# Kernel tuning notes

Measured on AMD Instinct MI355X. Metric: run time of the kernel, lower is better.

## Reference

```python
import jax, jax.numpy as jnp
import numpy as np

N, D = 8192, 256
NUM_CLASSES = 128
MARGIN = 0.2


def setup_inputs() -> dict:
    key = jax.random.key(0)
    k1, k2 = jax.random.split(key)
    embeddings = jax.random.normal(k1, (N, D), dtype=jnp.float32)
    labels = jax.random.randint(k2, (N,), 0, NUM_CLASSES, dtype=jnp.int64)
    return {"embeddings": embeddings, "labels": labels}


def reference(embeddings, labels):
    n = embeddings.shape[0]
    # cosine distance matrix: 1 - cos_sim, clipped to [0, 2]
    norm = jnp.sqrt(jnp.sum(embeddings * embeddings, axis=-1, keepdims=True))
    normed = embeddings / jnp.maximum(norm, 1e-12)
    sim = normed @ normed.T                      # (N, N)
    dist = jnp.clip(1.0 - sim, 0.0, 2.0)

    same = labels[:, None] == labels[None, :]    # (N, N) same-class mask
    eye = jnp.eye(n, dtype=bool)
    cand = same & ~eye                           # valid positives per anchor
    valid = cand.any(axis=1)                     # anchors with >=1 positive
    pos_idx = jnp.argmax(cand, axis=1)           # first same-class index != i

    rows = jnp.arange(n)
    d_ap = dist[rows, pos_idx]                   # (N,)

    # semi-hard mining: negatives with d_ap < d < d_ap + margin, fallback hardest
    neg = ~same                                  # different class (self excluded)
    semi = neg & (dist > d_ap[:, None]) & (dist < d_ap[:, None] + MARGIN)
    has_semi = semi.any(axis=1)
    inf = jnp.asarray(jnp.inf, dist.dtype)
    d_semi = jnp.where(semi, dist, inf)
    d_hard = jnp.where(neg, dist, inf)
    neg_idx = jnp.where(has_semi, jnp.argmin(d_semi, axis=1), jnp.argmin(d_hard, axis=1))

    d_an = dist[rows, neg_idx]
    losses = jnp.maximum(d_ap - d_an + MARGIN, 0.0) * valid.astype(dist.dtype)
    cnt = valid.sum().astype(dist.dtype)
    return jnp.where(cnt > 0, losses.sum() / cnt, jnp.zeros((), dist.dtype))
```

## Files before the change

### kernel.cpp

```cpp
#include <hip/hip_runtime.h>
#include <math.h>

#define NN 8192
#define DD 256
#define MARGIN 0.2f
#define SL 16
#define CPS (NN / SL)
#define TILES (CPS / 128)
#define IMAX 0x7fffffff

typedef __attribute__((ext_vector_type(4))) float f32x4;
typedef __attribute__((ext_vector_type(2))) long long2_t;
typedef unsigned int u32;
typedef unsigned short u16;
typedef unsigned char u8;

static __device__ __forceinline__ u8 f2e4m3(float x) {
    float a = fabsf(x);
    a = fminf(a, 448.0f);
    const u32 s = (__float_as_uint(x) >> 31) << 7;
    if (a < 0.015625f) {
        const int m = (int)rintf(a * 512.0f);
        return (u8)(s | m);
    }
    u32 u = __float_as_uint(a);
    u += 0x7FFFF + ((u >> 20) & 1);
    const u32 e = (u >> 23) - 120;
    return (u8)(s | (e << 3) | ((u >> 20) & 7));
}

#define GLOAD16(g, l)                                                             \
    __builtin_amdgcn_global_load_lds(                                             \
        (const __attribute__((address_space(1))) void*)(g),                       \
        (__attribute__((address_space(3))) void*)(l), 16, 0, 0)

static __device__ __forceinline__ void comb2(int& a1, int& a2, int b1, int b2) {
    const int lo = min(a1, b1);
    const int hi = max(a1, b1);
    a2 = min(hi, min(a2, b2));
    a1 = lo;
}

__global__ void kprepclass(const float* __restrict__ emb, const int* __restrict__ labels,
                           u8* __restrict__ E8, float* __restrict__ invn,
                           int* __restrict__ posidx) {
    const int tid = threadIdx.x;
    if (blockIdx.x < 2048) {
        const int wid = tid >> 6, l = tid & 63;
        const int row = blockIdx.x * 4 + wid;
        const float4 v = *(const float4*)&emb[(size_t)row * DD + l * 4];
        float ss = v.x * v.x + v.y * v.y + v.z * v.z + v.w * v.w;
#pragma unroll
        for (int o = 1; o < 64; o <<= 1) ss += __shfl_xor(ss, o);
        const float inv = 1.0f / fmaxf(sqrtf(ss), 1e-12f);
        if (l == 0) invn[row] = inv;
        const u32 b0 = f2e4m3(v.x * inv), b1 = f2e4m3(v.y * inv);
        const u32 b2 = f2e4m3(v.z * inv), b3 = f2e4m3(v.w * inv);
        const u32 packed = b0 | (b1 << 8) | (b2 << 16) | (b3 << 24);
        const int kc = l >> 4, h = (l >> 3) & 1, c = (l >> 1) & 3, o = (l & 1) * 4;
        const int g = kc * 64 + c * 16 + h * 8 + o;
        *(u32*)&E8[(size_t)row * DD + g] = packed;
    } else {
        const int c = blockIdx.x - 2048;
        int m1 = IMAX, m2 = IMAX;
        for (int j = tid; j < NN; j += 256) {
            if (labels[j] == c) {
                if (m1 == IMAX) m1 = j;
                else if (m2 == IMAX) m2 = j;
            }
        }
#pragma unroll
        for (int o = 1; o < 64; o <<= 1)
            comb2(m1, m2, __shfl_xor(m1, o), __shfl_xor(m2, o));
        __shared__ int s1[4], s2[4];
        __shared__ int bj1, bj2;
        const int wave = tid >> 6, lane = tid & 63;
        if (lane == 0) { s1[wave] = m1; s2[wave] = m2; }
        __syncthreads();
        if (tid == 0) {
            comb2(m1, m2, s1[1], s2[1]);
            comb2(m1, m2, s1[2], s2[2]);
            comb2(m1, m2, s1[3], s2[3]);
            bj1 = m1; bj2 = m2;
        }
        __syncthreads();
        const int j1 = bj1, j2 = bj2;
        for (int j = tid; j < NN; j += 256)
            if (labels[j] == c) posidx[j] = (j2 == IMAX) ? -1 : ((j == j1) ? j2 : j1);
    }
}

__global__ void kdap(const float* __restrict__ emb, const float* __restrict__ invn,
                     const int* __restrict__ posidx, float* __restrict__ dap) {
    const int wid = threadIdx.x >> 6, l = threadIdx.x & 63;
    const int i = blockIdx.x * 4 + wid;
    const int p = posidx[i];
    float dv = 0.0f;
    if (p >= 0) {
        const float4 a = *(const float4*)&emb[(size_t)i * DD + l * 4];
        const float4 b = *(const float4*)&emb[(size_t)p * DD + l * 4];
        float s = a.x * b.x + a.y * b.y + a.z * b.z + a.w * b.w;
#pragma unroll
        for (int o = 1; o < 64; o <<= 1) s += __shfl_xor(s, o);
        const float sim = s * invn[i] * invn[p];
        dv = fminf(fmaxf(1.0f - sim, 0.0f), 2.0f);
    }
    if (l == 0) dap[i] = dv;
}

__global__ __launch_bounds__(256) void kmine(
    const u8* __restrict__ E8, const int* __restrict__ labels,
    const float* __restrict__ dap, float* __restrict__ pM1, float* __restrict__ pMN)
{
    __shared__ __align__(16) u8 At0[128 * 256], At1[128 * 256];
    __shared__ __align__(16) int Ls[CPS];
    __shared__ float RedN[2][128], RedS[2][128];

    const int tid = threadIdx.x;
    const int l = tid & 63;
    const int wid = tid >> 6;
    const int wr = wid >> 1;
    const int wc = wid & 1;
    const int slice = blockIdx.x;
    const int a0 = blockIdx.y * 128;

    const int frow = l & 15;
    const int fq = l >> 4;

    if (tid < 128) {
        const int4 lv = *(const int4*)&labels[slice * CPS + tid * 4];
        *(int4*)&Ls[tid * 4] = lv;
    }
    int la[4]; float hiv[4];
#pragma unroll
    for (int n = 0; n < 4; ++n) {
        const int ai = a0 + wc * 64 + n * 16 + frow;
        la[n] = labels[ai];
        hiv[n] = 1.0f - dap[ai];
    }
    const char* Ec = (const char*)E8;
    long2_t breg[4][4];
#pragma unroll
    for (int n = 0; n < 4; ++n)
#pragma unroll
        for (int kc = 0; kc < 4; ++kc)
            breg[n][kc] = *(const long2_t*)(Ec +
                (size_t)(a0 + wc * 64 + n * 16 + frow) * 256 + kc * 64 + fq * 16);

    const char* asrc = Ec + ((size_t)(slice * CPS) + (tid >> 4)) * 256
                          + (((tid & 15) ^ (tid >> 4)) * 16);

#define STAGE(BUF, OFF) do {                                    \
        _Pragma("unroll")                                       \
        for (int i = 0; i < 8; ++i)                             \
            GLOAD16(asrc + (OFF) + i * 4096,                    \
                    &BUF[tid * 16 + i * 4096]);                 \
    } while (0)

    float mN[4], m1[4];
#pragma unroll
    for (int n = 0; n < 4; ++n) { mN[n] = -INFINITY; m1[n] = -INFINITY; }
    const f32x4 Zv = {0.f, 0.f, 0.f, 0.f};
    f32x4 acc[4][4];

#define COMPTILE(BUF, T) do {                                                       \
        _Pragma("unroll")                                                           \
        for (int kc = 0; kc < 4; ++kc) {                                            \
            long2_t a2[4];                                                          \
            _Pragma("unroll")                                                       \
            for (int m = 0; m < 4; ++m)                                             \
                a2[m] = *(const long2_t*)&BUF[(wr * 64 + m * 16 + frow) * 256       \
                                              + ((4 * kc + fq) ^ frow) * 16];      \
            __builtin_amdgcn_s_setprio(1);                                          \
            _Pragma("unroll")                                                       \
            for (int m = 0; m < 4; ++m)                                             \
                _Pragma("unroll")                                                   \
                for (int n = 0; n < 4; ++n)                                         \
                    acc[m][n] = __builtin_amdgcn_mfma_f32_16x16x32_fp8_fp8(         \
                        a2[m].x, breg[n][kc].x, (kc == 0) ? Zv : acc[m][n],         \
                        0, 0, 0);                                                   \
            _Pragma("unroll")                                                       \
            for (int m = 0; m < 4; ++m)                                             \
                _Pragma("unroll")                                                   \
                for (int n = 0; n < 4; ++n)                                         \
                    acc[m][n] = __builtin_amdgcn_mfma_f32_16x16x32_fp8_fp8(         \
                        a2[m].y, breg[n][kc].y, acc[m][n], 0, 0, 0);                \
            __builtin_amdgcn_s_setprio(0);                                          \
        }                                                                           \
        {                                                                           \
            int lcv[16];                                                            \
            _Pragma("unroll")                                                       \
            for (int m = 0; m < 4; ++m) {                                           \
                const int4 v = *(const int4*)&Ls[(T) * 128 + wr * 64 + m * 16       \
                                                 + fq * 4];                        \
                lcv[m * 4 + 0] = v.x; lcv[m * 4 + 1] = v.y;                         \
                lcv[m * 4 + 2] = v.z; lcv[m * 4 + 3] = v.w;                         \
            }                                                                       \
            _Pragma("unroll")                                                       \
            for (int n = 0; n < 4; ++n) {                                           \
                _Pragma("unroll")                                                   \
                for (int m = 0; m < 4; ++m)                                         \
                    _Pragma("unroll")                                               \
                    for (int r = 0; r < 4; ++r) {                                   \
                        const float sv = acc[m][n][r];                              \
                        const float sel = (lcv[m * 4 + r] != la[n]) ? sv            \
                                                                    : -INFINITY;    \
                        mN[n] = fmaxf(mN[n], sel);                                  \
                        m1[n] = fmaxf(m1[n], (sel < hiv[n]) ? sel : -INFINITY);     \
                    }                                                               \
            }                                                                       \
        }                                                                           \
    } while (0)

    STAGE(At0, 0);
    asm volatile("s_waitcnt lgkmcnt(0)" ::: "memory");

    STAGE(At1, 32768);
    asm volatile("s_waitcnt vmcnt(8)" ::: "memory");
    __builtin_amdgcn_s_barrier();
    COMPTILE(At0, 0);
    __builtin_amdgcn_s_barrier();
    STAGE(At0, 65536);
    asm volatile("s_waitcnt vmcnt(8)" ::: "memory");
    __builtin_amdgcn_s_barrier();
    COMPTILE(At1, 1);
    __builtin_amdgcn_s_barrier();
    STAGE(At1, 98304);
    asm volatile("s_waitcnt vmcnt(8)" ::: "memory");
    __builtin_amdgcn_s_barrier();
    COMPTILE(At0, 2);
    __builtin_amdgcn_s_barrier();
    asm volatile("s_waitcnt vmcnt(0)" ::: "memory");
    __builtin_amdgcn_s_barrier();
    COMPTILE(At1, 3);
#undef STAGE
#undef COMPTILE

#pragma unroll
    for (int n = 0; n < 4; ++n) {
        mN[n] = fmaxf(mN[n], __shfl_xor(mN[n], 16));
        mN[n] = fmaxf(mN[n], __shfl_xor(mN[n], 32));
        m1[n] = fmaxf(m1[n], __shfl_xor(m1[n], 16));
        m1[n] = fmaxf(m1[n], __shfl_xor(m1[n], 32));
    }
    __builtin_amdgcn_s_barrier();
    if (fq == 0) {
#pragma unroll
        for (int n = 0; n < 4; ++n) {
            RedN[wr][wc * 64 + n * 16 + frow] = mN[n];
            RedS[wr][wc * 64 + n * 16 + frow] = m1[n];
        }
    }
    __syncthreads();
    if (tid < 128) {
        pMN[slice * NN + a0 + tid] = fmaxf(RedN[0][tid], RedN[1][tid]);
        pM1[slice * NN + a0 + tid] = fmaxf(RedS[0][tid], RedS[1][tid]);
    }
}

__global__ void kcombine(const int* __restrict__ posidx, const float* __restrict__ dap,
                         const float* __restrict__ pM1, const float* __restrict__ pMN,
                         float* __restrict__ partials)
{
    const int i = blockIdx.x * 256 + threadIdx.x;
    float loss = 0.0f, cnt = 0.0f;
    if (posidx[i] >= 0) {
        float s1 = -INFINITY, sN = -INFINITY;
#pragma unroll
        for (int s = 0; s < SL; ++s) {
            s1 = fmaxf(s1, pM1[s * NN + i]);
            sN = fmaxf(sN, pMN[s * NN + i]);
        }
        const float da = dap[i];
        const float lo = 1.0f - da - MARGIN;
        const float M = (s1 > lo) ? s1 : sN;
        const float dan = fminf(fmaxf(1.0f - M, 0.0f), 2.0f);
        loss = fmaxf(da - dan + MARGIN, 0.0f);
        cnt = 1.0f;
    }
#pragma unroll
    for (int off = 1; off < 64; off <<= 1) {
        loss += __shfl_xor(loss, off);
        cnt  += __shfl_xor(cnt, off);
    }
    __shared__ float sl[4], sc[4];
    const int wave = threadIdx.x >> 6, lane = threadIdx.x & 63;
    if (lane == 0) { sl[wave] = loss; sc[wave] = cnt; }
    __syncthreads();
    if (threadIdx.x == 0) {
        partials[blockIdx.x]      = sl[0] + sl[1] + sl[2] + sl[3];
        partials[32 + blockIdx.x] = sc[0] + sc[1] + sc[2] + sc[3];
    }
}

__global__ void kfinal(const float* __restrict__ partials, float* __restrict__ out) {
    const int t = threadIdx.x;
    float L = (t < 32) ? partials[t] : 0.0f;
    float C = (t < 32) ? partials[32 + t] : 0.0f;
#pragma unroll
    for (int off = 1; off < 64; off <<= 1) {
        L += __shfl_xor(L, off);
        C += __shfl_xor(C, off);
    }
    if (t == 0) out[0] = (C > 0.0f) ? (L / C) : 0.0f;
}

extern "C" void kernel_launch(void* const* d_in, const int* in_sizes, int n_in,
                              void* d_out, int out_size, void* d_ws, size_t ws_size,
                              hipStream_t stream) {
    const float* emb  = (const float*)d_in[0];
    const int* labels = (const int*)d_in[1];
    float* out = (float*)d_out;

    char* w = (char*)d_ws;
    u8*    E8   = (u8*)w;                        w += (size_t)NN * DD;
    float* invn = (float*)w;                     w += NN * 4;
    float* dapv = (float*)w;                     w += NN * 4;
    int*   posi = (int*)w;                       w += NN * 4;
    float* pM1  = (float*)w;                     w += (size_t)SL * NN * 4;
    float* pMN  = (float*)w;                     w += (size_t)SL * NN * 4;
    float* parts = (float*)w;

    kprepclass<<<2048 + 128, 256, 0, stream>>>(emb, labels, E8, invn, posi);
    kdap<<<NN / 4, 256, 0, stream>>>(emb, invn, posi, dapv);
    kmine<<<dim3(SL, NN / 128), 256, 0, stream>>>(E8, labels, dapv, pM1, pMN);
    kcombine<<<NN / 256, 256, 0, stream>>>(posi, dapv, pM1, pMN, parts);
    kfinal<<<1, 64, 0, stream>>>(parts, out);
}
```

Before: 58.17 us.

## Use 16x16x128 scaled FP8 MFMA and fold final reduction into combine kernel

Replaces the pairs of 16x16x32 FP8 MFMAs with a single MX-scaled 16x16x128 f8f6f4 MFMA per K half, using unit scales. To feed the wider operands it drops the interleaved E8 layout for a plain row layout and loads 32 contiguous bytes per operand. It also removes the separate final-reduction launch: the last combine block to finish, detected with an atomic counter, performs the final sum. This cuts MFMA instruction count and one kernel launch, but needs a counter reset in the prep kernel and changes the LDS read pattern.

```diff
diff --git a/kernel.cpp b/kernel.cpp
--- a/kernel.cpp
+++ b/kernel.cpp
@@ -11,8 +11,8 @@
 
 typedef __attribute__((ext_vector_type(4))) float f32x4;
 typedef __attribute__((ext_vector_type(2))) long long2_t;
+typedef __attribute__((ext_vector_type(8))) int i32x8;
 typedef unsigned int u32;
-typedef unsigned short u16;
 typedef unsigned char u8;
 
 static __device__ __forceinline__ u8 f2e4m3(float x) {
@@ -29,6 +29,12 @@
     return (u8)(s | (e << 3) | ((u >> 20) & 7));
 }
 
+static __device__ __forceinline__ i32x8 pack8(long2_t lo, long2_t hi) {
+    union { long2_t l2[2]; i32x8 v; } u;
+    u.l2[0] = lo; u.l2[1] = hi;
+    return u.v;
+}
+
 #define GLOAD16(g, l)                                                             \
     __builtin_amdgcn_global_load_lds(                                             \
         (const __attribute__((address_space(1))) void*)(g),                       \
@@ -43,7 +49,7 @@
 
 __global__ void kprepclass(const float* __restrict__ emb, const int* __restrict__ labels,
                            u8* __restrict__ E8, float* __restrict__ invn,
-                           int* __restrict__ posidx) {
+                           int* __restrict__ posidx, u32* __restrict__ cnt_done) {
     const int tid = threadIdx.x;
     if (blockIdx.x < 2048) {
         const int wid = tid >> 6, l = tid & 63;
@@ -57,11 +63,10 @@
         const u32 b0 = f2e4m3(v.x * inv), b1 = f2e4m3(v.y * inv);
         const u32 b2 = f2e4m3(v.z * inv), b3 = f2e4m3(v.w * inv);
         const u32 packed = b0 | (b1 << 8) | (b2 << 16) | (b3 << 24);
-        const int kc = l >> 4, h = (l >> 3) & 1, c = (l >> 1) & 3, o = (l & 1) * 4;
-        const int g = kc * 64 + c * 16 + h * 8 + o;
-        *(u32*)&E8[(size_t)row * DD + g] = packed;
+        *(u32*)&E8[(size_t)row * DD + l * 4] = packed;
     } else {
         const int c = blockIdx.x - 2048;
+        if (c == 0 && tid == 0) *cnt_done = 0;
         int m1 = IMAX, m2 = IMAX;
         for (int j = tid; j < NN; j += 256) {
             if (labels[j] == c) {
@@ -139,13 +144,15 @@
         hiv[n] = 1.0f - dap[ai];
     }
     const char* Ec = (const char*)E8;
-    long2_t breg[4][4];
+    i32x8 breg[4][2];
 #pragma unroll
     for (int n = 0; n < 4; ++n)
 #pragma unroll
-        for (int kc = 0; kc < 4; ++kc)
-            breg[n][kc] = *(const long2_t*)(Ec +
-                (size_t)(a0 + wc * 64 + n * 16 + frow) * 256 + kc * 64 + fq * 16);
+        for (int kh = 0; kh < 2; ++kh) {
+            const char* p = Ec + (size_t)(a0 + wc * 64 + n * 16 + frow) * 256
+                               + kh * 128 + fq * 32;
+            breg[n][kh] = pack8(*(const long2_t*)p, *(const long2_t*)(p + 16));
+        }
 
     const char* asrc = Ec + ((size_t)(slice * CPS) + (tid >> 4)) * 256
                           + (((tid & 15) ^ (tid >> 4)) * 16);
@@ -165,26 +172,25 @@
 
 #define COMPTILE(BUF, T) do {                                                       \
         _Pragma("unroll")                                                           \
-        for (int kc = 0; kc < 4; ++kc) {                                            \
-            long2_t a2[4];                                                          \
+        for (int kh = 0; kh < 2; ++kh) {                                            \
+            i32x8 a8[4];                                                            \
             _Pragma("unroll")                                                       \
-            for (int m = 0; m < 4; ++m)                                             \
-                a2[m] = *(const long2_t*)&BUF[(wr * 64 + m * 16 + frow) * 256       \
-                                              + ((4 * kc + fq) ^ frow) * 16];      \
+            for (int m = 0; m < 4; ++m) {                                           \
+                const int row = wr * 64 + m * 16 + frow;                            \
+                const int cb = kh * 8 + fq * 2;                                     \
+                const int p0 = (cb ^ (row & 15)) * 16;                              \
+                const int p1 = ((cb + 1) ^ (row & 15)) * 16;                        \
+                a8[m] = pack8(*(const long2_t*)&BUF[row * 256 + p0],                \
+                              *(const long2_t*)&BUF[row * 256 + p1]);               \
+            }                                                                       \
             __builtin_amdgcn_s_setprio(1);                                          \
             _Pragma("unroll")                                                       \
             for (int m = 0; m < 4; ++m)                                             \
                 _Pragma("unroll")                                                   \
                 for (int n = 0; n < 4; ++n)                                         \
-                    acc[m][n] = __builtin_amdgcn_mfma_f32_16x16x32_fp8_fp8(         \
-                        a2[m].x, breg[n][kc].x, (kc == 0) ? Zv : acc[m][n],         \
-                        0, 0, 0);                                                   \
-            _Pragma("unroll")                                                       \
-            for (int m = 0; m < 4; ++m)                                             \
-                _Pragma("unroll")                                                   \
-                for (int n = 0; n < 4; ++n)                                         \
-                    acc[m][n] = __builtin_amdgcn_mfma_f32_16x16x32_fp8_fp8(         \
-                        a2[m].y, breg[n][kc].y, acc[m][n], 0, 0, 0);                \
+                    acc[m][n] = __builtin_amdgcn_mfma_scale_f32_16x16x128_f8f6f4(   \
+                        a8[m], breg[n][kh], (kh == 0) ? Zv : acc[m][n],             \
+                        0, 0, 0, 0x7F7F7F7F, 0, 0x7F7F7F7F);                        \
             __builtin_amdgcn_s_setprio(0);                                          \
         }                                                                           \
         {                                                                           \
@@ -260,7 +266,8 @@
 
 __global__ void kcombine(const int* __restrict__ posidx, const float* __restrict__ dap,
                          const float* __restrict__ pM1, const float* __restrict__ pMN,
-                         float* __restrict__ partials)
+                         float* __restrict__ partials, u32* __restrict__ cnt_done,
+                         float* __restrict__ out)
 {
     const int i = blockIdx.x * 256 + threadIdx.x;
     float loss = 0.0f, cnt = 0.0f;
@@ -284,25 +291,28 @@
         cnt  += __shfl_xor(cnt, off);
     }
     __shared__ float sl[4], sc[4];
+    __shared__ int last;
     const int wave = threadIdx.x >> 6, lane = threadIdx.x & 63;
     if (lane == 0) { sl[wave] = loss; sc[wave] = cnt; }
     __syncthreads();
     if (threadIdx.x == 0) {
         partials[blockIdx.x]      = sl[0] + sl[1] + sl[2] + sl[3];
         partials[32 + blockIdx.x] = sc[0] + sc[1] + sc[2] + sc[3];
-    }
-}
-
-__global__ void kfinal(const float* __restrict__ partials, float* __restrict__ out) {
-    const int t = threadIdx.x;
-    float L = (t < 32) ? partials[t] : 0.0f;
-    float C = (t < 32) ? partials[32 + t] : 0.0f;
-#pragma unroll
-    for (int off = 1; off < 64; off <<= 1) {
-        L += __shfl_xor(L, off);
-        C += __shfl_xor(C, off);
-    }
-    if (t == 0) out[0] = (C > 0.0f) ? (L / C) : 0.0f;
+        __threadfence();
+        last = (atomicAdd(cnt_done, 1u) == 31u);
+    }
+    __syncthreads();
+    if (last && threadIdx.x < 64) {
+        const int t = threadIdx.x;
+        float L = (t < 32) ? partials[t] : 0.0f;
+        float C = (t < 32) ? partials[32 + t] : 0.0f;
+#pragma unroll
+        for (int off = 1; off < 64; off <<= 1) {
+            L += __shfl_xor(L, off);
+            C += __shfl_xor(C, off);
+        }
+        if (t == 0) out[0] = (C > 0.0f) ? (L / C) : 0.0f;
+    }
 }
 
 extern "C" void kernel_launch(void* const* d_in, const int* in_sizes, int n_in,
@@ -319,11 +329,11 @@
     int*   posi = (int*)w;                       w += NN * 4;
     float* pM1  = (float*)w;                     w += (size_t)SL * NN * 4;
     float* pMN  = (float*)w;                     w += (size_t)SL * NN * 4;
-    float* parts = (float*)w;
-
-    kprepclass<<<2048 + 128, 256, 0, stream>>>(emb, labels, E8, invn, posi);
+    float* parts = (float*)w;                    w += 64 * 4;
+    u32*   cdone = (u32*)w;
+
+    kprepclass<<<2048 + 128, 256, 0, stream>>>(emb, labels, E8, invn, posi, cdone);
     kdap<<<NN / 4, 256, 0, stream>>>(emb, invn, posi, dapv);
     kmine<<<dim3(SL, NN / 128), 256, 0, stream>>>(E8, labels, dapv, pM1, pMN);
-    kcombine<<<NN / 256, 256, 0, stream>>>(posi, dapv, pM1, pMN, parts);
-    kfinal<<<1, 64, 0, stream>>>(parts, out);
-}
+    kcombine<<<NN / 256, 256, 0, stream>>>(posi, dapv, pM1, pMN, parts, cdone, out);
+}
```

Result: faster. 54.74 us (-5.9%).
